# Performance work log

Hardware: AMD Instinct MI355X
Metric: run time of the kernel (lower is better)

## Reference

```python
import jax, jax.numpy as jnp
import numpy as np

EMBED = 512
HEADS = 8
HIDDEN = 4 * EMBED
EPS = 1e-5


def setup_inputs() -> dict:
    key = jax.random.key(0)
    ks = jax.random.split(key, 12)
    s = lambda fan_in: 1.0 / np.sqrt(fan_in)
    return {
        "x": jax.random.normal(ks[0], (4, 2048, EMBED), dtype=jnp.float32),
        "ln1_g": jnp.ones((EMBED,), jnp.float32),
        "ln1_b": jnp.zeros((EMBED,), jnp.float32),
        "qkv_w": jax.random.uniform(ks[1], (EMBED, 3 * EMBED), jnp.float32, -s(EMBED), s(EMBED)),
        "qkv_b": jax.random.uniform(ks[2], (3 * EMBED,), jnp.float32, -s(EMBED), s(EMBED)),
        "proj_w": jax.random.uniform(ks[3], (EMBED, EMBED), jnp.float32, -s(EMBED), s(EMBED)),
        "proj_b": jax.random.uniform(ks[4], (EMBED,), jnp.float32, -s(EMBED), s(EMBED)),
        "ln2_g": jnp.ones((EMBED,), jnp.float32),
        "ln2_b": jnp.zeros((EMBED,), jnp.float32),
        "fc1_w": jax.random.uniform(ks[5], (EMBED, HIDDEN), jnp.float32, -s(EMBED), s(EMBED)),
        "fc1_b": jax.random.uniform(ks[6], (HIDDEN,), jnp.float32, -s(EMBED), s(EMBED)),
        "fc2_w": jax.random.uniform(ks[7], (HIDDEN, EMBED), jnp.float32, -s(HIDDEN), s(HIDDEN)),
        "fc2_b": jax.random.uniform(ks[8], (EMBED,), jnp.float32, -s(HIDDEN), s(HIDDEN)),
    }


def _layernorm(x, g, b):
    mu = jnp.mean(x, axis=-1, keepdims=True)
    var = jnp.mean(jnp.square(x - mu), axis=-1, keepdims=True)
    return (x - mu) * jax.lax.rsqrt(var + EPS) * g + b


def reference(x, ln1_g, ln1_b, qkv_w, qkv_b, proj_w, proj_b,
              ln2_g, ln2_b, fc1_w, fc1_b, fc2_w, fc2_b):
    B, N, C = x.shape
    H, D = HEADS, C // HEADS
    scale = D ** -0.5

    # --- attention sub-block (pre-LN) ---
    h = _layernorm(x, ln1_g, ln1_b)
    qkv = h @ qkv_w + qkv_b                      # [B,N,3C]
    q, k, v = jnp.split(qkv, 3, axis=-1)
    q = q.reshape(B, N, H, D).transpose(0, 2, 1, 3)  # [B,H,N,D]
    k = k.reshape(B, N, H, D).transpose(0, 2, 1, 3)
    v = v.reshape(B, N, H, D).transpose(0, 2, 1, 3)
    attn = jnp.einsum('bhqd,bhkd->bhqk', q, k) * scale
    attn = jax.nn.softmax(attn, axis=-1)
    o = jnp.einsum('bhqk,bhkd->bhqd', attn, v)
    o = o.transpose(0, 2, 1, 3).reshape(B, N, C)
    x = x + (o @ proj_w + proj_b)

    # --- MLP sub-block (pre-LN, exact GELU) ---
    h = _layernorm(x, ln2_g, ln2_b)
    h = jax.nn.gelu(h @ fc1_w + fc1_b, approximate=False)
    x = x + (h @ fc2_w + fc2_b)
    return x
```

## Files before the change

kernel.cpp:

```cpp
#include <hip/hip_runtime.h>
#include <math.h>


using bf16x8 = __attribute__((ext_vector_type(8))) short;
using f32x4  = __attribute__((ext_vector_type(4))) float;

typedef unsigned short u16;
typedef unsigned int   u32;

__device__ __forceinline__ u16 f2bf(float f) {
    u32 u; __builtin_memcpy(&u, &f, 4);
    u32 r = u + 0x7FFFu + ((u >> 16) & 1u);
    return (u16)(r >> 16);
}
__device__ __forceinline__ u32 fbits(float f) {
    u32 u; __builtin_memcpy(&u, &f, 4); return u;
}
__device__ __forceinline__ float f_from_bits(u32 u) {
    float f; __builtin_memcpy(&f, &u, 4); return f;
}
__device__ __forceinline__ u32 pack_trunc(float lo, float hi) {
    return __builtin_amdgcn_perm(fbits(hi), fbits(lo), 0x07060302u);
}
__device__ __forceinline__ u32 pack_rne(float lo, float hi) {
    return (u32)f2bf(lo) | ((u32)f2bf(hi) << 16);
}
__device__ __forceinline__ void gload16(const void* g, void* l) {
    __builtin_amdgcn_global_load_lds(
        (const __attribute__((address_space(1))) unsigned int*)g,
        (__attribute__((address_space(3))) unsigned int*)l, 16, 0, 0);
}

__global__ __launch_bounds__(256) void k_pre(
        const float* __restrict__ w0, u16* __restrict__ d0,
        const float* __restrict__ w1, u16* __restrict__ d1,
        const float* __restrict__ w2, u16* __restrict__ d2,
        const float* __restrict__ w3, u16* __restrict__ d3,
        const float* __restrict__ x, const float* __restrict__ g,
        const float* __restrict__ bta, u16* __restrict__ hout) {
    __shared__ float tile[32][33];
    const int bid = blockIdx.x;
    if (bid < 3072) {
        const float* w; u16* dst; int K, N, tb;
        if (bid < 768)       { w = w0; dst = d0; K = 512;  N = 1536; tb = bid; }
        else if (bid < 1024) { w = w1; dst = d1; K = 512;  N = 512;  tb = bid - 768; }
        else if (bid < 2048) { w = w2; dst = d2; K = 512;  N = 2048; tb = bid - 1024; }
        else                 { w = w3; dst = d3; K = 2048; N = 512;  tb = bid - 2048; }
        const int nb = N >> 5;
        const int k0 = (tb / nb) << 5;
        const int n0 = (tb % nb) << 5;
        const int c = threadIdx.x & 31, r = threadIdx.x >> 5;
#pragma unroll
        for (int i = 0; i < 4; i++)
            tile[r + i * 8][c] = w[(size_t)(k0 + r + i * 8) * N + n0 + c];
        __syncthreads();
#pragma unroll
        for (int i = 0; i < 4; i++)
            dst[(size_t)(n0 + r + i * 8) * K + k0 + c] = f2bf(tile[c][r + i * 8]);
    } else {
        const int row  = ((bid - 3072) << 2) + (threadIdx.x >> 6);
        const int lane = threadIdx.x & 63;
        const float* xr = x + (size_t)row * 512 + lane * 8;
        float4 a = *(const float4*)xr;
        float4 c = *(const float4*)(xr + 4);
        float s = a.x + a.y + a.z + a.w + c.x + c.y + c.z + c.w;
        float q = a.x*a.x + a.y*a.y + a.z*a.z + a.w*a.w
                + c.x*c.x + c.y*c.y + c.z*c.z + c.w*c.w;
#pragma unroll
        for (int off = 32; off; off >>= 1) {
            s += __shfl_xor(s, off, 64);
            q += __shfl_xor(q, off, 64);
        }
        const float mean = s * (1.0f / 512.0f);
        const float var  = q * (1.0f / 512.0f) - mean * mean;
        const float rstd = rsqrtf(var + 1e-5f);
        float vv[8] = {a.x, a.y, a.z, a.w, c.x, c.y, c.z, c.w};
        const int col0 = lane * 8;
        u32 ov[4];
#pragma unroll
        for (int j = 0; j < 4; j++) {
            const float lo = (vv[2*j]   - mean) * rstd * g[col0+2*j]   + bta[col0+2*j];
            const float hi = (vv[2*j+1] - mean) * rstd * g[col0+2*j+1] + bta[col0+2*j+1];
            ov[j] = pack_rne(lo, hi);
        }
        *(uint4*)(hout + (size_t)row * 512 + col0) = make_uint4(ov[0], ov[1], ov[2], ov[3]);
    }
}

__global__ __launch_bounds__(256) void k_ln(const float* __restrict__ x,
                                            const float* __restrict__ g,
                                            const float* __restrict__ bta,
                                            u16* __restrict__ out) {
    const int row  = (blockIdx.x << 2) + (threadIdx.x >> 6);
    const int lane = threadIdx.x & 63;
    const float* xr = x + (size_t)row * 512 + lane * 8;
    float4 a = *(const float4*)xr;
    float4 c = *(const float4*)(xr + 4);
    float s = a.x + a.y + a.z + a.w + c.x + c.y + c.z + c.w;
    float q = a.x*a.x + a.y*a.y + a.z*a.z + a.w*a.w
            + c.x*c.x + c.y*c.y + c.z*c.z + c.w*c.w;
#pragma unroll
    for (int off = 32; off; off >>= 1) {
        s += __shfl_xor(s, off, 64);
        q += __shfl_xor(q, off, 64);
    }
    const float mean = s * (1.0f / 512.0f);
    const float var  = q * (1.0f / 512.0f) - mean * mean;
    const float rstd = rsqrtf(var + 1e-5f);
    float vv[8] = {a.x, a.y, a.z, a.w, c.x, c.y, c.z, c.w};
    const int col0 = lane * 8;
    u32 ov[4];
#pragma unroll
    for (int j = 0; j < 4; j++) {
        const float lo = (vv[2*j]   - mean) * rstd * g[col0+2*j]   + bta[col0+2*j];
        const float hi = (vv[2*j+1] - mean) * rstd * g[col0+2*j+1] + bta[col0+2*j+1];
        ov[j] = pack_rne(lo, hi);
    }
    *(uint4*)(out + (size_t)row * 512 + col0) = make_uint4(ov[0], ov[1], ov[2], ov[3]);
}

template <int EP, int TN>
__global__ __launch_bounds__(256, 3) void k_gemm(const u16* __restrict__ A,
                                                 const u16* __restrict__ Bt,
                                                 const float* __restrict__ bias,
                                                 const float* __restrict__ res,
                                                 float* __restrict__ outF,
                                                 u16* __restrict__ outB,
                                                 u16* __restrict__ out2,
                                                 int M, int N, int K) {
    constexpr int NT = TN / 32;
    __shared__ u16 As[128 * 64];
    __shared__ u16 Bs[TN * 64];
    const int nb = N / TN;
    const int xg = blockIdx.x & 7, sg = blockIdx.x >> 3;
    const int m0 = ((sg / nb) * 8 + xg) << 7;
    const int n0 = (sg % nb) * TN;
    const int t = threadIdx.x, lane = t & 63, w = t >> 6;
    const int wr = (w >> 1) << 6;
    const int wc = (w & 1) * (TN / 2);
    const int quad = lane >> 4, l15 = lane & 15;
    const int x7 = l15 & 7;
    const bool vpart = (EP == 3) && (n0 >= 1024);

    f32x4 acc[4][NT];
#pragma unroll
    for (int i = 0; i < 4; i++)
#pragma unroll
        for (int j = 0; j < NT; j++) acc[i][j] = (f32x4){0.f, 0.f, 0.f, 0.f};

    const size_t Kb = (size_t)K * 2;
    const char* ga = (const char*)A + (size_t)m0 * Kb;
    const char* gb = (const char*)Bt + (size_t)n0 * Kb;
    const int o0 = t * 16;

    for (int k0 = 0; k0 < K; k0 += 64) {
        const int kb = k0 * 2;
#pragma unroll
        for (int i = 0; i < 4; i++) {
            const int o4 = i * 4096 + o0;
            const int row = o4 >> 7;
            const int lc = ((o4 >> 4) & 7) ^ (row & 7);
            gload16(ga + (size_t)row * Kb + kb + lc * 16, (char*)As + o4);
        }
#pragma unroll
        for (int i = 0; i < TN / 32; i++) {
            const int o4 = i * 4096 + o0;
            const int row = o4 >> 7;
            const int lc = ((o4 >> 4) & 7) ^ (row & 7);
            gload16(gb + (size_t)row * Kb + kb + lc * 16, (char*)Bs + o4);
        }
        __syncthreads();
#pragma unroll
        for (int ks = 0; ks < 2; ks++) {
            const int cidx = ((ks * 4 + quad) ^ x7) * 8;
            bf16x8 af[4], bfr[NT];
#pragma unroll
            for (int i = 0; i < 4; i++)
                af[i] = *(const bf16x8*)(As + (wr + i * 16 + l15) * 64 + cidx);
#pragma unroll
            for (int j = 0; j < NT; j++)
                bfr[j] = *(const bf16x8*)(Bs + (wc + j * 16 + l15) * 64 + cidx);
            if (vpart) {
#pragma unroll
                for (int mt = 0; mt < 4; mt++)
#pragma unroll
                    for (int nt = 0; nt < NT; nt++)
                        acc[mt][nt] = __builtin_amdgcn_mfma_f32_16x16x32_bf16(
                            af[mt], bfr[nt], acc[mt][nt], 0, 0, 0);
            } else {
#pragma unroll
                for (int mt = 0; mt < 4; mt++)
#pragma unroll
                    for (int nt = 0; nt < NT; nt++)
                        acc[mt][nt] = __builtin_amdgcn_mfma_f32_16x16x32_bf16(
                            bfr[nt], af[mt], acc[mt][nt], 0, 0, 0);
            }
        }
        __syncthreads();
    }

    if (vpart) {
#pragma unroll
        for (int mt = 0; mt < 4; mt++)
#pragma unroll
            for (int nt = 0; nt < NT; nt++) {
                const int col = n0 + wc + nt * 16 + l15;
                const float bi = bias[col];
                const int row0 = m0 + wr + mt * 16 + quad * 4;
                const int b = row0 >> 11, key = row0 & 2047;
                const int hd = col - 1024;
                u32 p0 = pack_rne(acc[mt][nt][0] + bi, acc[mt][nt][1] + bi);
                u32 p1 = pack_rne(acc[mt][nt][2] + bi, acc[mt][nt][3] + bi);
                *(uint2*)(out2 + (size_t)(b * 512 + hd) * 2048 + key) = make_uint2(p0, p1);
            }
    } else {
        const bool qpart = (EP == 3) && (n0 < 512);
#pragma unroll
        for (int mt = 0; mt < 4; mt++) {
            const int row = m0 + wr + mt * 16 + l15;
#pragma unroll
            for (int nt = 0; nt < NT; nt++) {
                const int c4 = n0 + wc + nt * 16 + quad * 4;
                const float4 b4 = *(const float4*)(bias + c4);
                float v[4];
#pragma unroll
                for (int r = 0; r < 4; r++) {
                    v[r] = acc[mt][nt][r] + ((const float*)&b4)[r];
                    if (EP == 1) {
                        float y = v[r] * (0.79788456f + 0.035677408f * v[r] * v[r]);
                        y = fminf(y, 40.0f);
                        float tE = exp2f(y * 2.88539008f);
                        v[r] = v[r] * tE * __builtin_amdgcn_rcpf(tE + 1.0f);
                    }
                    if (qpart) v[r] *= 0.18033688f;
                }
                const size_t oi = (size_t)row * N + c4;
                if (EP == 2) {
                    const float4 r4 = *(const float4*)(res + oi);
                    float4 o4v = make_float4(v[0] + r4.x, v[1] + r4.y,
                                             v[2] + r4.z, v[3] + r4.w);
                    *(float4*)(outF + oi) = o4v;
                } else {
                    *(uint2*)(outB + oi) =
                        make_uint2(pack_rne(v[0], v[1]), pack_rne(v[2], v[3]));
                }
            }
        }
    }
}

__global__ __launch_bounds__(256, 4) void k_attn(const u16* __restrict__ qkv,
                                                 const u16* __restrict__ vt,
                                                 u16* __restrict__ po0,
                                                 u16* __restrict__ po1,
                                                 float* __restrict__ pden) {
    __shared__ u16 smem[16384];
    u16* Ks = smem;
    u16* Vs = smem + 4096;
    u16* Psw = smem + 8192;
    u16* Qs = smem;
    const int bid = blockIdx.x;
    const int h = bid & 7, sg = bid >> 3;
    const int qt = sg & 15, kh = (sg >> 4) & 1, b = sg >> 5;
    const int q0 = qt << 7;
    const int t = threadIdx.x, lane = t & 63, w = t >> 6;
    const int quad = lane >> 4, l15 = lane & 15;
    const int x7 = l15 & 7;

    const char* gq = (const char*)qkv + (size_t)((b << 11) + q0) * 3072 + h * 128;
    const char* gk = (const char*)qkv + (size_t)((b << 11) + (kh << 10)) * 3072 + 1024 + h * 128;
    const char* gv = (const char*)vt + (size_t)((b << 3) + h) * 64 * 4096 + (kh << 10) * 2;

#pragma unroll
    for (int i = 0; i < 4; i++) {
        const int o4 = i * 4096 + t * 16;
        const int row = o4 >> 7;
        const int lc = ((o4 >> 4) & 7) ^ (row & 7);
        gload16(gq + (size_t)row * 3072 + lc * 16, (char*)Qs + o4);
    }
    __syncthreads();

    bf16x8 qf[2][2];
#pragma unroll
    for (int ks = 0; ks < 2; ks++) {
        const int cidx = ((ks * 4 + quad) ^ x7) * 8;
#pragma unroll
        for (int nt = 0; nt < 2; nt++)
            qf[ks][nt] = *(const bf16x8*)(Qs + (w * 32 + nt * 16 + l15) * 64 + cidx);
    }
    __syncthreads();

    f32x4 accO[4][2];
    float denp[2] = {0.f, 0.f};
#pragma unroll
    for (int mt = 0; mt < 4; mt++)
#pragma unroll
        for (int nt = 0; nt < 2; nt++) accO[mt][nt] = (f32x4){0.f, 0.f, 0.f, 0.f};

    for (int kt = 0; kt < 16; kt++) {
        const int kk = kt << 6;
#pragma unroll
        for (int i = 0; i < 2; i++) {
            const int o4 = i * 4096 + t * 16;
            const int row = o4 >> 7;
            const int lc = ((o4 >> 4) & 7) ^ (row & 7);
            gload16(gk + (size_t)(kk + row) * 3072 + lc * 16, (char*)Ks + o4);
            gload16(gv + (size_t)row * 4096 + kk * 2 + lc * 16, (char*)Vs + o4);
        }
        __syncthreads();

        f32x4 s[4][2];
#pragma unroll
        for (int mt = 0; mt < 4; mt++)
#pragma unroll
            for (int nt = 0; nt < 2; nt++) s[mt][nt] = (f32x4){0.f, 0.f, 0.f, 0.f};
#pragma unroll
        for (int ks = 0; ks < 2; ks++) {
            const int cidx = ((ks * 4 + quad) ^ x7) * 8;
            bf16x8 kf[4];
#pragma unroll
            for (int mt = 0; mt < 4; mt++)
                kf[mt] = *(const bf16x8*)(Ks + (mt * 16 + l15) * 64 + cidx);
#pragma unroll
            for (int mt = 0; mt < 4; mt++)
#pragma unroll
                for (int nt = 0; nt < 2; nt++)
                    s[mt][nt] = __builtin_amdgcn_mfma_f32_16x16x32_bf16(
                        kf[mt], qf[ks][nt], s[mt][nt], 0, 0, 0);
        }

#pragma unroll
        for (int mt = 0; mt < 4; mt++)
#pragma unroll
            for (int nt = 0; nt < 2; nt++) {
                const float p0 = exp2f(s[mt][nt][0]);
                const float p1 = exp2f(s[mt][nt][1]);
                const float p2 = exp2f(s[mt][nt][2]);
                const float p3 = exp2f(s[mt][nt][3]);
                denp[nt] += (p0 + p1) + (p2 + p3);
                const u32 d0 = pack_trunc(p0, p1);
                const u32 d1 = pack_trunc(p2, p3);
                const int pidx = (nt * 16 + l15) * 64 +
                                 (((2 * mt + (quad >> 1)) ^ x7) << 3) + (quad & 1) * 4;
                *(uint2*)(&Psw[w * 2048 + pidx]) = make_uint2(d0, d1);
            }

#pragma unroll
        for (int ks = 0; ks < 2; ks++) {
            const int cidx = ((ks * 4 + quad) ^ x7) * 8;
            bf16x8 vf[4], pf[2];
#pragma unroll
            for (int mt = 0; mt < 4; mt++)
                vf[mt] = *(const bf16x8*)(Vs + (mt * 16 + l15) * 64 + cidx);
#pragma unroll
            for (int nt = 0; nt < 2; nt++)
                pf[nt] = *(const bf16x8*)(Psw + w * 2048 + (nt * 16 + l15) * 64 + cidx);
#pragma unroll
            for (int mt = 0; mt < 4; mt++)
#pragma unroll
                for (int nt = 0; nt < 2; nt++)
                    accO[mt][nt] = __builtin_amdgcn_mfma_f32_16x16x32_bf16(
                        vf[mt], pf[nt], accO[mt][nt], 0, 0, 0);
        }
        __syncthreads();
    }

    u16* po = kh ? po1 : po0;
#pragma unroll
    for (int nt = 0; nt < 2; nt++) {
        float dn = denp[nt];
        dn += __shfl_xor(dn, 16, 64);
        dn += __shfl_xor(dn, 32, 64);
        if (quad == 0)
            pden[(size_t)(((kh << 5) + (b << 3) + h) << 11) + q0 + w * 32 + nt * 16 + l15] = dn;
#pragma unroll
        for (int mt = 0; mt < 4; mt++) {
            const int qg = q0 + w * 32 + nt * 16 + l15;
            const u32 p0 = pack_rne(accO[mt][nt][0], accO[mt][nt][1]);
            const u32 p1 = pack_rne(accO[mt][nt][2], accO[mt][nt][3]);
            *(uint2*)(po + (size_t)((b << 11) + qg) * 512 + h * 64 + mt * 16 + quad * 4) =
                make_uint2(p0, p1);
        }
    }
}

__global__ __launch_bounds__(256) void k_combine(u16* __restrict__ po0,
                                                 const u16* __restrict__ po1,
                                                 const float* __restrict__ pden) {
    const int idx8 = (blockIdx.x * 256 + threadIdx.x) * 8;
    const int row = idx8 >> 9, col = idx8 & 511;
    const int h = col >> 6, q = row & 2047, b = row >> 11;
    const size_t di = (size_t)(((b << 3) + h) << 11) + q;
    const float den = pden[di] + pden[di + (32 << 11)];
    const float r = __builtin_amdgcn_rcpf(den);
    uint4 a = *(const uint4*)(po0 + idx8);
    uint4 c = *(const uint4*)(po1 + idx8);
    u32 av[4] = {a.x, a.y, a.z, a.w}, cv[4] = {c.x, c.y, c.z, c.w}, ov[4];
#pragma unroll
    for (int i = 0; i < 4; i++) {
        const float lo = (f_from_bits(av[i] << 16) + f_from_bits(cv[i] << 16)) * r;
        const float hi = (f_from_bits(av[i] & 0xFFFF0000u) +
                          f_from_bits(cv[i] & 0xFFFF0000u)) * r;
        ov[i] = pack_rne(lo, hi);
    }
    *(uint4*)(po0 + idx8) = make_uint4(ov[0], ov[1], ov[2], ov[3]);
}

extern "C" void kernel_launch(void* const* d_in, const int* in_sizes, int n_in,
                              void* d_out, int out_size, void* d_ws, size_t ws_size,
                              hipStream_t stream) {
    const float* x      = (const float*)d_in[0];
    const float* ln1_g  = (const float*)d_in[1];
    const float* ln1_b  = (const float*)d_in[2];
    const float* qkv_w  = (const float*)d_in[3];
    const float* qkv_b  = (const float*)d_in[4];
    const float* proj_w = (const float*)d_in[5];
    const float* proj_b = (const float*)d_in[6];
    const float* ln2_g  = (const float*)d_in[7];
    const float* ln2_b  = (const float*)d_in[8];
    const float* fc1_w  = (const float*)d_in[9];
    const float* fc1_b  = (const float*)d_in[10];
    const float* fc2_w  = (const float*)d_in[11];
    const float* fc2_b  = (const float*)d_in[12];
    float* out = (float*)d_out;
    char* ws = (char*)d_ws;

    u16*   qkv_wT = (u16*)(ws + 0);
    u16*   proj_wT= (u16*)(ws + 1572864);
    u16*   fc1_wT = (u16*)(ws + 2097152);
    u16*   fc2_wT = (u16*)(ws + 4194304);
    u16*   h      = (u16*)(ws + 6291456);
    float* pden   = (float*)(ws + 6291456);
    u16*   qkv    = (u16*)(ws + 14680064);
    u16*   vt     = (u16*)(ws + 39845888);
    u16*   o      = (u16*)(ws + 48234496);
    u16*   po1    = (u16*)(ws + 56623104);
    float* x1     = (float*)(ws + 56623104);
    u16*   f1     = (u16*)(ws + 14680064);
    u16*   h2     = h;

    k_pre<<<5120, 256, 0, stream>>>(qkv_w, qkv_wT, proj_w, proj_wT,
                                    fc1_w, fc1_wT, fc2_w, fc2_wT,
                                    x, ln1_g, ln1_b, h);
    k_gemm<3,128><<<(8192/128)*(1536/128), 256, 0, stream>>>(
        h, qkv_wT, qkv_b, nullptr, nullptr, qkv, vt, 8192, 1536, 512);
    k_attn<<<1024, 256, 0, stream>>>(qkv, vt, o, po1, pden);
    k_combine<<<2048, 256, 0, stream>>>(o, po1, pden);
    k_gemm<2,64><<<(8192/128)*(512/64), 256, 0, stream>>>(
        o, proj_wT, proj_b, x, x1, nullptr, nullptr, 8192, 512, 512);
    k_ln<<<2048, 256, 0, stream>>>(x1, ln2_g, ln2_b, h2);
    k_gemm<1,128><<<(8192/128)*(2048/128), 256, 0, stream>>>(
        h2, fc1_wT, fc1_b, nullptr, nullptr, f1, nullptr, 8192, 2048, 512);
    k_gemm<2,64><<<(8192/128)*(512/64), 256, 0, stream>>>(
        f1, fc2_wT, fc2_b, x1, out, nullptr, nullptr, 8192, 512, 2048);
}
```

Measured before the change: 281.6 us.

## Use two-wave attention blocks with 64 query rows per wave and unify GEMM epilogue

```diff
diff --git a/kernel.cpp b/kernel.cpp
--- a/kernel.cpp
+++ b/kernel.cpp
@@ -140,7 +140,6 @@
     const int wc = (w & 1) * (TN / 2);
     const int quad = lane >> 4, l15 = lane & 15;
     const int x7 = l15 & 7;
-    const bool vpart = (EP == 3) && (n0 >= 1024);
 
     f32x4 acc[4][NT];
 #pragma unroll
@@ -180,76 +179,52 @@
 #pragma unroll
             for (int j = 0; j < NT; j++)
                 bfr[j] = *(const bf16x8*)(Bs + (wc + j * 16 + l15) * 64 + cidx);
+#pragma unroll
+            for (int mt = 0; mt < 4; mt++)
+#pragma unroll
+                for (int nt = 0; nt < NT; nt++)
+                    acc[mt][nt] = __builtin_amdgcn_mfma_f32_16x16x32_bf16(
+                        af[mt], bfr[nt], acc[mt][nt], 0, 0, 0);
+        }
+        __syncthreads();
+    }
+
+    const bool vpart = (EP == 3) && (n0 >= 1024);
+    const bool qpart = (EP == 3) && (n0 < 512);
+#pragma unroll
+    for (int mt = 0; mt < 4; mt++)
+#pragma unroll
+        for (int nt = 0; nt < NT; nt++) {
+            const int col = n0 + wc + nt * 16 + l15;
+            const float bi = bias[col];
+            const int row0 = m0 + wr + mt * 16 + quad * 4;
             if (vpart) {
-#pragma unroll
-                for (int mt = 0; mt < 4; mt++)
-#pragma unroll
-                    for (int nt = 0; nt < NT; nt++)
-                        acc[mt][nt] = __builtin_amdgcn_mfma_f32_16x16x32_bf16(
-                            af[mt], bfr[nt], acc[mt][nt], 0, 0, 0);
-            } else {
-#pragma unroll
-                for (int mt = 0; mt < 4; mt++)
-#pragma unroll
-                    for (int nt = 0; nt < NT; nt++)
-                        acc[mt][nt] = __builtin_amdgcn_mfma_f32_16x16x32_bf16(
-                            bfr[nt], af[mt], acc[mt][nt], 0, 0, 0);
-            }
-        }
-        __syncthreads();
-    }
-
-    if (vpart) {
-#pragma unroll
-        for (int mt = 0; mt < 4; mt++)
-#pragma unroll
-            for (int nt = 0; nt < NT; nt++) {
-                const int col = n0 + wc + nt * 16 + l15;
-                const float bi = bias[col];
-                const int row0 = m0 + wr + mt * 16 + quad * 4;
                 const int b = row0 >> 11, key = row0 & 2047;
                 const int hd = col - 1024;
                 u32 p0 = pack_rne(acc[mt][nt][0] + bi, acc[mt][nt][1] + bi);
                 u32 p1 = pack_rne(acc[mt][nt][2] + bi, acc[mt][nt][3] + bi);
                 *(uint2*)(out2 + (size_t)(b * 512 + hd) * 2048 + key) = make_uint2(p0, p1);
-            }
-    } else {
-        const bool qpart = (EP == 3) && (n0 < 512);
-#pragma unroll
-        for (int mt = 0; mt < 4; mt++) {
-            const int row = m0 + wr + mt * 16 + l15;
-#pragma unroll
-            for (int nt = 0; nt < NT; nt++) {
-                const int c4 = n0 + wc + nt * 16 + quad * 4;
-                const float4 b4 = *(const float4*)(bias + c4);
-                float v[4];
+            } else {
 #pragma unroll
                 for (int r = 0; r < 4; r++) {
-                    v[r] = acc[mt][nt][r] + ((const float*)&b4)[r];
+                    const int row = row0 + r;
+                    float v = acc[mt][nt][r] + bi;
+                    const size_t oi = (size_t)row * N + col;
                     if (EP == 1) {
-                        float y = v[r] * (0.79788456f + 0.035677408f * v[r] * v[r]);
+                        float y = v * (0.79788456f + 0.035677408f * v * v);
                         y = fminf(y, 40.0f);
                         float tE = exp2f(y * 2.88539008f);
-                        v[r] = v[r] * tE * __builtin_amdgcn_rcpf(tE + 1.0f);
+                        v = v * tE * __builtin_amdgcn_rcpf(tE + 1.0f);
                     }
-                    if (qpart) v[r] *= 0.18033688f;
-                }
-                const size_t oi = (size_t)row * N + c4;
-                if (EP == 2) {
-                    const float4 r4 = *(const float4*)(res + oi);
-                    float4 o4v = make_float4(v[0] + r4.x, v[1] + r4.y,
-                                             v[2] + r4.z, v[3] + r4.w);
-                    *(float4*)(outF + oi) = o4v;
-                } else {
-                    *(uint2*)(outB + oi) =
-                        make_uint2(pack_rne(v[0], v[1]), pack_rne(v[2], v[3]));
+                    if (qpart) v *= 0.18033688f;
+                    if (EP == 2) outF[oi] = v + res[oi];
+                    else         outB[oi] = f2bf(v);
                 }
             }
         }
-    }
-}
-
-__global__ __launch_bounds__(256, 4) void k_attn(const u16* __restrict__ qkv,
+}
+
+__global__ __launch_bounds__(128, 2) void k_attn(const u16* __restrict__ qkv,
                                                  const u16* __restrict__ vt,
                                                  u16* __restrict__ po0,
                                                  u16* __restrict__ po1,
@@ -272,36 +247,36 @@
     const char* gv = (const char*)vt + (size_t)((b << 3) + h) * 64 * 4096 + (kh << 10) * 2;
 
 #pragma unroll
-    for (int i = 0; i < 4; i++) {
-        const int o4 = i * 4096 + t * 16;
+    for (int i = 0; i < 8; i++) {
+        const int o4 = i * 2048 + t * 16;
         const int row = o4 >> 7;
         const int lc = ((o4 >> 4) & 7) ^ (row & 7);
         gload16(gq + (size_t)row * 3072 + lc * 16, (char*)Qs + o4);
     }
     __syncthreads();
 
-    bf16x8 qf[2][2];
+    bf16x8 qf[2][4];
 #pragma unroll
     for (int ks = 0; ks < 2; ks++) {
         const int cidx = ((ks * 4 + quad) ^ x7) * 8;
 #pragma unroll
-        for (int nt = 0; nt < 2; nt++)
-            qf[ks][nt] = *(const bf16x8*)(Qs + (w * 32 + nt * 16 + l15) * 64 + cidx);
+        for (int nt = 0; nt < 4; nt++)
+            qf[ks][nt] = *(const bf16x8*)(Qs + (w * 64 + nt * 16 + l15) * 64 + cidx);
     }
     __syncthreads();
 
-    f32x4 accO[4][2];
-    float denp[2] = {0.f, 0.f};
+    f32x4 accO[4][4];
+    float denp[4] = {0.f, 0.f, 0.f, 0.f};
 #pragma unroll
     for (int mt = 0; mt < 4; mt++)
 #pragma unroll
-        for (int nt = 0; nt < 2; nt++) accO[mt][nt] = (f32x4){0.f, 0.f, 0.f, 0.f};
+        for (int nt = 0; nt < 4; nt++) accO[mt][nt] = (f32x4){0.f, 0.f, 0.f, 0.f};
 
     for (int kt = 0; kt < 16; kt++) {
         const int kk = kt << 6;
 #pragma unroll
-        for (int i = 0; i < 2; i++) {
-            const int o4 = i * 4096 + t * 16;
+        for (int i = 0; i < 4; i++) {
+            const int o4 = i * 2048 + t * 16;
             const int row = o4 >> 7;
             const int lc = ((o4 >> 4) & 7) ^ (row & 7);
             gload16(gk + (size_t)(kk + row) * 3072 + lc * 16, (char*)Ks + o4);
@@ -309,73 +284,65 @@
         }
         __syncthreads();
 
-        f32x4 s[4][2];
-#pragma unroll
-        for (int mt = 0; mt < 4; mt++)
-#pragma unroll
-            for (int nt = 0; nt < 2; nt++) s[mt][nt] = (f32x4){0.f, 0.f, 0.f, 0.f};
-#pragma unroll
-        for (int ks = 0; ks < 2; ks++) {
-            const int cidx = ((ks * 4 + quad) ^ x7) * 8;
-            bf16x8 kf[4];
-#pragma unroll
-            for (int mt = 0; mt < 4; mt++)
-                kf[mt] = *(const bf16x8*)(Ks + (mt * 16 + l15) * 64 + cidx);
-#pragma unroll
-            for (int mt = 0; mt < 4; mt++)
-#pragma unroll
-                for (int nt = 0; nt < 2; nt++)
-                    s[mt][nt] = __builtin_amdgcn_mfma_f32_16x16x32_bf16(
-                        kf[mt], qf[ks][nt], s[mt][nt], 0, 0, 0);
-        }
-
-#pragma unroll
-        for (int mt = 0; mt < 4; mt++)
-#pragma unroll
-            for (int nt = 0; nt < 2; nt++) {
-                const float p0 = exp2f(s[mt][nt][0]);
-                const float p1 = exp2f(s[mt][nt][1]);
-                const float p2 = exp2f(s[mt][nt][2]);
-                const float p3 = exp2f(s[mt][nt][3]);
+#pragma unroll
+        for (int mt = 0; mt < 4; mt++) {
+            f32x4 s[4];
+#pragma unroll
+            for (int nt = 0; nt < 4; nt++) s[nt] = (f32x4){0.f, 0.f, 0.f, 0.f};
+#pragma unroll
+            for (int ks = 0; ks < 2; ks++) {
+                const int cidx = ((ks * 4 + quad) ^ x7) * 8;
+                const bf16x8 kf = *(const bf16x8*)(Ks + (mt * 16 + l15) * 64 + cidx);
+#pragma unroll
+                for (int nt = 0; nt < 4; nt++)
+                    s[nt] = __builtin_amdgcn_mfma_f32_16x16x32_bf16(
+                        kf, qf[ks][nt], s[nt], 0, 0, 0);
+            }
+#pragma unroll
+            for (int nt = 0; nt < 4; nt++) {
+                const float p0 = exp2f(s[nt][0]);
+                const float p1 = exp2f(s[nt][1]);
+                const float p2 = exp2f(s[nt][2]);
+                const float p3 = exp2f(s[nt][3]);
                 denp[nt] += (p0 + p1) + (p2 + p3);
                 const u32 d0 = pack_trunc(p0, p1);
                 const u32 d1 = pack_trunc(p2, p3);
                 const int pidx = (nt * 16 + l15) * 64 +
                                  (((2 * mt + (quad >> 1)) ^ x7) << 3) + (quad & 1) * 4;
-                *(uint2*)(&Psw[w * 2048 + pidx]) = make_uint2(d0, d1);
+                *(uint2*)(&Psw[w * 4096 + pidx]) = make_uint2(d0, d1);
             }
+        }
 
 #pragma unroll
         for (int ks = 0; ks < 2; ks++) {
             const int cidx = ((ks * 4 + quad) ^ x7) * 8;
-            bf16x8 vf[4], pf[2];
-#pragma unroll
-            for (int mt = 0; mt < 4; mt++)
-                vf[mt] = *(const bf16x8*)(Vs + (mt * 16 + l15) * 64 + cidx);
-#pragma unroll
-            for (int nt = 0; nt < 2; nt++)
-                pf[nt] = *(const bf16x8*)(Psw + w * 2048 + (nt * 16 + l15) * 64 + cidx);
-#pragma unroll
-            for (int mt = 0; mt < 4; mt++)
-#pragma unroll
-                for (int nt = 0; nt < 2; nt++)
+            bf16x8 pf[4];
+#pragma unroll
+            for (int nt = 0; nt < 4; nt++)
+                pf[nt] = *(const bf16x8*)(Psw + w * 4096 + (nt * 16 + l15) * 64 + cidx);
+#pragma unroll
+            for (int mt = 0; mt < 4; mt++) {
+                const bf16x8 vf = *(const bf16x8*)(Vs + (mt * 16 + l15) * 64 + cidx);
+#pragma unroll
+                for (int nt = 0; nt < 4; nt++)
                     accO[mt][nt] = __builtin_amdgcn_mfma_f32_16x16x32_bf16(
-                        vf[mt], pf[nt], accO[mt][nt], 0, 0, 0);
+                        vf, pf[nt], accO[mt][nt], 0, 0, 0);
+            }
         }
         __syncthreads();
     }
 
     u16* po = kh ? po1 : po0;
 #pragma unroll
-    for (int nt = 0; nt < 2; nt++) {
+    for (int nt = 0; nt < 4; nt++) {
         float dn = denp[nt];
         dn += __shfl_xor(dn, 16, 64);
         dn += __shfl_xor(dn, 32, 64);
+        const int qg = q0 + w * 64 + nt * 16 + l15;
         if (quad == 0)
-            pden[(size_t)(((kh << 5) + (b << 3) + h) << 11) + q0 + w * 32 + nt * 16 + l15] = dn;
+            pden[(size_t)(((kh << 5) + (b << 3) + h) << 11) + qg] = dn;
 #pragma unroll
         for (int mt = 0; mt < 4; mt++) {
-            const int qg = q0 + w * 32 + nt * 16 + l15;
             const u32 p0 = pack_rne(accO[mt][nt][0], accO[mt][nt][1]);
             const u32 p1 = pack_rne(accO[mt][nt][2], accO[mt][nt][3]);
             *(uint2*)(po + (size_t)((b << 11) + qg) * 512 + h * 64 + mt * 16 + quad * 4) =
@@ -444,7 +411,7 @@
                                     x, ln1_g, ln1_b, h);
     k_gemm<3,128><<<(8192/128)*(1536/128), 256, 0, stream>>>(
         h, qkv_wT, qkv_b, nullptr, nullptr, qkv, vt, 8192, 1536, 512);
-    k_attn<<<1024, 256, 0, stream>>>(qkv, vt, o, po1, pden);
+    k_attn<<<1024, 128, 0, stream>>>(qkv, vt, o, po1, pden);
     k_combine<<<2048, 256, 0, stream>>>(o, po1, pden);
     k_gemm<2,64><<<(8192/128)*(512/64), 256, 0, stream>>>(
         o, proj_wT, proj_b, x, x1, nullptr, nullptr, 8192, 512, 512);
```

Measured after the change: 269.0 us. 1.05x faster.
